# Optimization experiments

Measured on AMD Instinct MI355X. Metric: run time of the kernel, lower is better.

## Reference

```python
import jax, jax.numpy as jnp
import numpy as np

B, T_IN, T_OUT, F, H = 256, 336, 96, 32, 256


def _lstm_cell(x_t, h, c, Wih, Whh, b):
    # PyTorch gate order: input, forget, cell(g), output
    gates = x_t @ Wih.T + h @ Whh.T + b  # [B, 4H]
    i, f, g, o = jnp.split(gates, 4, axis=-1)
    c_new = jax.nn.sigmoid(f) * c + jax.nn.sigmoid(i) * jnp.tanh(g)
    h_new = jax.nn.sigmoid(o) * jnp.tanh(c_new)
    return h_new, c_new


def setup_inputs() -> dict:
    key = jax.random.key(0)
    ks = jax.random.split(key, 16)
    s = 0.05  # keep recurrence numerically tame
    g = lambda k, shape: (jax.random.normal(k, shape) * s).astype(jnp.float32)
    return {
        "x": jax.random.normal(ks[0], (B, T_IN, F), dtype=jnp.float32),
        "enc_Wih0": g(ks[1], (4 * H, F)),
        "enc_Whh0": g(ks[2], (4 * H, H)),
        "enc_b0": g(ks[3], (4 * H,)),
        "enc_Wih1": g(ks[4], (4 * H, H)),
        "enc_Whh1": g(ks[5], (4 * H, H)),
        "enc_b1": g(ks[6], (4 * H,)),
        "dec_Wih0": g(ks[7], (4 * H, F)),
        "dec_Whh0": g(ks[8], (4 * H, H)),
        "dec_b0": g(ks[9], (4 * H,)),
        "dec_Wih1": g(ks[10], (4 * H, H)),
        "dec_Whh1": g(ks[11], (4 * H, H)),
        "dec_b1": g(ks[12], (4 * H,)),
        "dec_Wout": g(ks[13], (F, H)),
        "dec_bout": g(ks[14], (F,)),
    }


def reference(x, enc_Wih0, enc_Whh0, enc_b0, enc_Wih1, enc_Whh1, enc_b1,
              dec_Wih0, dec_Whh0, dec_b0, dec_Wih1, dec_Whh1, dec_b1,
              dec_Wout, dec_bout):
    batch = x.shape[0]
    zeros = jnp.zeros((batch, H), dtype=x.dtype)

    # --- encoder: step-by-step 2-layer LSTM over input sequence ---
    def enc_step(carry, x_t):
        h0, c0, h1, c1 = carry
        h0, c0 = _lstm_cell(x_t, h0, c0, enc_Wih0, enc_Whh0, enc_b0)
        h1, c1 = _lstm_cell(h0, h1, c1, enc_Wih1, enc_Whh1, enc_b1)
        return (h0, c0, h1, c1), None

    xs = jnp.swapaxes(x, 0, 1)  # [T_IN, B, F]
    (h0, c0, h1, c1), _ = jax.lax.scan(enc_step, (zeros, zeros, zeros, zeros), xs)

    def dec_step(carry, _):
        h0, c0, h1, c1, y = carry
        h0, c0 = _lstm_cell(y, h0, c0, dec_Wih0, dec_Whh0, dec_b0)
        h1, c1 = _lstm_cell(h0, h1, c1, dec_Wih1, dec_Whh1, dec_b1)
        y = h1 @ dec_Wout.T + dec_bout  # project hidden -> feature dim
        return (h0, c0, h1, c1, y), y

    y0 = x[:, -1, :]  # [B, F]
    _, ys = jax.lax.scan(dec_step, (h0, c0, h1, c1, y0), None, length=T_OUT)
    return jnp.swapaxes(ys, 0, 1)  # [B, T_OUT, F]
```

## Files before the change

kernel.cpp:

```cpp
#include <hip/hip_runtime.h>
#include <hip/hip_bf16.h>

#define BB   256
#define TIN  336
#define TOUT 96
#define FF   32
#define HH   256

#define NGS 16
#define NBG 16
#define RPG 16
#define TPB 512

#define KB0 9
#define KB1 16
#define ASTRIDE 520
#define XSTRIDE 40

#define N_L0  (16*4*KB0*64*8)
#define N_L1  (16*4*KB1*64*8)
#define U_E0  0
#define U_E1  (U_E0 + N_L0)
#define U_D0  (U_E1 + N_L1)
#define U_D1  (U_D0 + N_L1)
#define U_END (U_D1 + N_L1)
#define HPAR  65536
#define U_H0  U_END
#define U_H1  (U_H0 + 2*HPAR)
#define U_HD  (U_H1 + 2*HPAR)
#define U_CTR (U_HD + 96*HPAR)
#define U_ZEND (U_CTR + 2048)

#define GATE(bias, g, r, cc) (bias[(g)*16 + (cc)] + pbuf[0][r][(g)*16 + (cc)] + pbuf[1][r][(g)*16 + (cc)])

typedef __bf16 bf16x8 __attribute__((ext_vector_type(8)));
typedef float  f32x4  __attribute__((ext_vector_type(4)));

__device__ __forceinline__ float sigf(float x) { return 1.f / (1.f + __expf(-x)); }
__device__ __forceinline__ float tanhfast(float x) { return 1.f - 2.f / (__expf(2.f * x) + 1.f); }
__device__ __forceinline__ unsigned short f2bf(float f) {
    union { float f; unsigned u; } v; v.f = f;
    unsigned r = v.u + 0x7FFF + ((v.u >> 16) & 1);
    return (unsigned short)(r >> 16);
}
__device__ __forceinline__ uint4 ldg_sc(const void* p) {
    uint4 v;
    asm volatile("global_load_dwordx4 %0, %1, off sc0 sc1\n\ts_waitcnt vmcnt(0)"
                 : "=v"(v) : "v"(p) : "memory");
    return v;
}
__device__ __forceinline__ void ldg_sc2(const void* p0, const void* p1, uint4& a, uint4& b) {
    asm volatile("global_load_dwordx4 %0, %2, off sc0 sc1\n\t"
                 "global_load_dwordx4 %1, %3, off sc0 sc1\n\t"
                 "s_waitcnt vmcnt(0)"
                 : "=v"(a), "=v"(b) : "v"(p0), "v"(p1) : "memory");
}

__global__ void prep_kernel(const float* __restrict__ eWih0, const float* __restrict__ eWhh0,
                            const float* __restrict__ eWih1, const float* __restrict__ eWhh1,
                            const float* __restrict__ dWih0, const float* __restrict__ dWhh0,
                            const float* __restrict__ dWih1, const float* __restrict__ dWhh1,
                            const float* __restrict__ Wout,  float* __restrict__ wsf)
{
    unsigned short* wsu = (unsigned short*)wsf;
    for (long u = (long)blockIdx.x * blockDim.x + threadIdx.x; u < (long)U_END;
         u += (long)gridDim.x * blockDim.x) {
        int region; long l;
        if (u < U_E1)      { region = 0; l = u - U_E0; }
        else if (u < U_D0) { region = 1; l = u - U_E1; }
        else if (u < U_D1) { region = 2; l = u - U_D0; }
        else               { region = 3; l = u - U_D1; }
        const int KB = (region == 0) ? KB0 : KB1;
        int j = (int)(l & 7), lane = (int)((l >> 3) & 63);
        long rem = l >> 9;
        int kb = (int)(rem % KB), q = (int)(rem / KB);
        int nt = q & 3, gi = q >> 2;
        int k  = kb * 32 + ((lane >> 4) << 3) + j;
        int gj = nt * 256 + gi * 16 + (lane & 15);
        float v;
        if (region == 0)      v = (k < 32)  ? eWih0[gj * 32 + k]  : eWhh0[gj * 256 + (k - 32)];
        else if (region == 1) v = (k < 256) ? eWih1[gj * 256 + k] : eWhh1[gj * 256 + (k - 256)];
        else if (region == 2) {
            if (k < 256) v = dWhh0[gj * 256 + k];
            else {
                float acc = 0.f; int kk = k - 256;
                #pragma unroll 8
                for (int f = 0; f < 32; ++f) acc += dWih0[gj * 32 + f] * Wout[f * 256 + kk];
                v = acc;
            }
        } else                v = (k < 256) ? dWih1[gj * 256 + k] : dWhh1[gj * 256 + (k - 256)];
        wsu[u] = f2bf(v);
    }
    for (long z = (long)blockIdx.x * blockDim.x + threadIdx.x; z < (long)(4 * HPAR);
         z += (long)gridDim.x * blockDim.x)
        wsu[U_H0 + z] = 0;
    for (long z = (long)blockIdx.x * blockDim.x + threadIdx.x; z < 2048;
         z += (long)gridDim.x * blockDim.x)
        wsu[U_CTR + z] = 0;
}

__global__ __launch_bounds__(TPB) void lstm_main(
    const float* __restrict__ x,
    const float* __restrict__ eb0, const float* __restrict__ eb1,
    const float* __restrict__ db0, const float* __restrict__ db1,
    const float* __restrict__ Wout, const float* __restrict__ bout,
    const float* __restrict__ dWih0,
    float* __restrict__ ws, float* __restrict__ out)
{
    const int gi = blockIdx.x >> 4;
    const int gb = blockIdx.x & 15;

    unsigned short* wsu = (unsigned short*)ws;
    const unsigned short* h0u = wsu + U_H0;
    const unsigned short* h1u = wsu + U_H1;
    const unsigned short* hdu = wsu + U_HD;
    unsigned* h0d = (unsigned*)(wsu + U_H0);
    unsigned* hdd = (unsigned*)(wsu + U_HD);
    unsigned* flg = (unsigned*)(wsu + U_CTR) + gb * 32;

    const int t  = threadIdx.x;
    const int wv = t >> 6;
    const int ln = t & 63;
    const int nt = wv & 3, w2 = wv >> 2;
    const int arow = ln & 15, ak = (ln >> 4) << 3;

    __shared__ __align__(16) unsigned short Atile[16 * ASTRIDE];
    __shared__ __align__(16) unsigned short Xtile[16 * XSTRIDE];
    __shared__ float pbuf[2][16][68];
    __shared__ float cst[2][16][16];
    __shared__ float sb[5][64];

    if (t < 64) {
        int gj = (t >> 4) * 256 + gi * 16 + (t & 15);
        sb[0][t] = eb0[gj]; sb[1][t] = eb1[gj]; sb[3][t] = db1[gj]; sb[4][t] = db0[gj];
        float be = db0[gj];
        #pragma unroll 8
        for (int f = 0; f < 32; ++f) be += dWih0[gj * 32 + f] * bout[f];
        sb[2][t] = be;
    }
    if (t < 256) { cst[0][t >> 4][t & 15] = 0.f; cst[1][t >> 4][t & 15] = 0.f; }

    bf16x8 B0[8], B1[8];
    const int kbs0 = w2 ? 4 : 0, kbn0 = w2 ? 5 : 4;
    const int kbs1 = w2 ? 8 : 0;
    auto loadB = [&](size_t ubase, int KB, int kbs, int kbn, bf16x8* Breg) {
        #pragma unroll
        for (int i = 0; i < 8; ++i)
            if (i < kbn)
                Breg[i] = *(const bf16x8*)(wsu + ubase +
                            ((size_t)(nt * KB + kbs + i) * 64 + ln) * 8);
    };

    int posts = 0;
    auto gsync = [&]() {
        ++posts;
        if (t == 0)
            __hip_atomic_store(flg + gi, (unsigned)posts, __ATOMIC_RELAXED,
                               __HIP_MEMORY_SCOPE_AGENT);
        if (wv == 0) {
            for (;;) {
                unsigned v = __hip_atomic_load(flg + (ln & 15), __ATOMIC_RELAXED,
                                               __HIP_MEMORY_SCOPE_AGENT);
                if (__all((int)(v >= (unsigned)posts))) break;
                __builtin_amdgcn_s_sleep(1);
            }
        }
        __syncthreads();
    };

    auto stageEnc = [&](const unsigned short* h0src, const unsigned short* h1src, int xs) {
        const int r = t >> 5, c8 = t & 31;
        uint4 a, b;
        ldg_sc2(h0src + (size_t)(gb * RPG + r) * 256 + c8 * 8,
                h1src + (size_t)(gb * RPG + r) * 256 + c8 * 8, a, b);
        float xv = 0.f;
        if (xs >= 0) xv = x[((size_t)(gb * RPG + r) * TIN + xs) * FF + c8];
        *(uint4*)(Atile + r * ASTRIDE + c8 * 8) = a;
        *(uint4*)(Atile + r * ASTRIDE + 256 + c8 * 8) = b;
        if (xs >= 0) Xtile[r * XSTRIDE + c8] = f2bf(xv);
    };
    auto stageOne = [&](const unsigned short* src, int colbase) {
        const int r = t >> 5, c8 = t & 31;
        uint4 a = ldg_sc(src + (size_t)(gb * RPG + r) * 256 + c8 * 8);
        *(uint4*)(Atile + r * ASTRIDE + colbase + c8 * 8) = a;
    };
    auto stageTwo = [&](const unsigned short* s0, int cb0, const unsigned short* s1, int cb1) {
        const int r = t >> 5, c8 = t & 31;
        uint4 a, b;
        ldg_sc2(s0 + (size_t)(gb * RPG + r) * 256 + c8 * 8,
                s1 + (size_t)(gb * RPG + r) * 256 + c8 * 8, a, b);
        *(uint4*)(Atile + r * ASTRIDE + cb0 + c8 * 8) = a;
        *(uint4*)(Atile + r * ASTRIDE + cb1 + c8 * 8) = b;
    };
    auto stageZero = [&](int colbase) {
        const int r = t >> 5, c8 = t & 31;
        uint4 z = {0u, 0u, 0u, 0u};
        *(uint4*)(Atile + r * ASTRIDE + colbase + c8 * 8) = z;
    };

    auto phase = [&](const bf16x8* Breg, int kbs, int kbn, bool withX, const float* bias,
                     int layer, unsigned* hdstDw, bool addY0) {
        f32x4 acc = {0.f, 0.f, 0.f, 0.f};
        #pragma unroll
        for (int i = 0; i < 8; ++i) {
            if (i < kbn) {
                const int kb = kbs + i;
                bf16x8 a;
                if (withX && kb == 0) a = *(const bf16x8*)(Xtile + arow * XSTRIDE + ak);
                else {
                    const int koff = (withX ? (kb - 1) : kb) * 32;
                    a = *(const bf16x8*)(Atile + arow * ASTRIDE + koff + ak);
                }
                acc = __builtin_amdgcn_mfma_f32_16x16x32_bf16(a, Breg[i], acc, 0, 0, 0);
            }
        }
        #pragma unroll
        for (int rg = 0; rg < 4; ++rg)
            pbuf[w2][(ln >> 4) * 4 + rg][nt * 16 + arow] = acc[rg];
        __syncthreads();
        if (t < 128) {
            const int r = t >> 3, c2 = t & 7;
            const int c0 = c2 * 2, c1 = c0 + 1;
            float xi0 = GATE(bias, 0, r, c0), xf0 = GATE(bias, 1, r, c0);
            float xg0 = GATE(bias, 2, r, c0), xo0 = GATE(bias, 3, r, c0);
            float xi1 = GATE(bias, 0, r, c1), xf1 = GATE(bias, 1, r, c1);
            float xg1 = GATE(bias, 2, r, c1), xo1 = GATE(bias, 3, r, c1);
            if (addY0) {
                const float* xp = x + ((size_t)(gb * RPG + r) * TIN + (TIN - 1)) * FF;
                float xr[32];
                #pragma unroll
                for (int f = 0; f < 32; ++f) xr[f] = xp[f];
                #pragma unroll
                for (int g = 0; g < 4; ++g) {
                    const float* w0 = dWih0 + (size_t)(g * 256 + gi * 16 + c0) * 32;
                    const float* w1 = dWih0 + (size_t)(g * 256 + gi * 16 + c1) * 32;
                    float a0 = 0.f, a1 = 0.f;
                    #pragma unroll
                    for (int f = 0; f < 32; ++f) {
                        a0 = fmaf(w0[f], xr[f], a0);
                        a1 = fmaf(w1[f], xr[f], a1);
                    }
                    if (g == 0) { xi0 += a0; xi1 += a1; }
                    else if (g == 1) { xf0 += a0; xf1 += a1; }
                    else if (g == 2) { xg0 += a0; xg1 += a1; }
                    else { xo0 += a0; xo1 += a1; }
                }
            }
            float ca = cst[layer][r][c0], cb = cst[layer][r][c1];
            float cn0 = sigf(xf0) * ca + sigf(xi0) * tanhfast(xg0);
            float cn1 = sigf(xf1) * cb + sigf(xi1) * tanhfast(xg1);
            cst[layer][r][c0] = cn0; cst[layer][r][c1] = cn1;
            float h0v = sigf(xo0) * tanhfast(cn0);
            float h1v = sigf(xo1) * tanhfast(cn1);
            unsigned pv = (unsigned)f2bf(h0v) | ((unsigned)f2bf(h1v) << 16);
            __hip_atomic_store(hdstDw + (size_t)(gb * RPG + r) * 128 + gi * 8 + c2, pv,
                               __ATOMIC_RELAXED, __HIP_MEMORY_SCOPE_AGENT);
        }
        __syncthreads();
    };

    loadB(U_E0 + (size_t)gi * 18432, KB0, kbs0, kbn0, B0);
    loadB(U_E1 + (size_t)gi * 32768, KB1, kbs1, 8,    B1);
    { const int r = t >> 5, c8 = t & 31;
      uint4 z = {0u, 0u, 0u, 0u};
      *(uint4*)(Atile + r * ASTRIDE + c8 * 8) = z;
      Xtile[r * XSTRIDE + c8] = f2bf(x[((size_t)(gb * RPG + r) * TIN) * FF + c8]); }
    __syncthreads();

    for (int s = 0; s < TIN; ++s) {
        const int rp = s & 1, wp = rp ^ 1;
        phase(B0, kbs0, kbn0, true, sb[0], 0, h0d + (size_t)wp * (HPAR / 2), false);
        gsync();
        stageEnc(h0u + (size_t)wp * HPAR, h1u + (size_t)rp * HPAR,
                 (s + 1 < TIN) ? s + 1 : -1);
        __syncthreads();
        phase(B1, kbs1, 8, false, sb[1], 1,
              (unsigned*)(wsu + U_H1) + (size_t)wp * (HPAR / 2), false);
    }

    loadB(U_D0 + (size_t)gi * 32768, KB1, kbs1, 8, B0);
    loadB(U_D1 + (size_t)gi * 32768, KB1, kbs1, 8, B1);

    for (int s = TIN; s < TIN + TOUT; ++s) {
        const int wp = (s & 1) ^ 1, td = s - TIN;
        gsync();
        if (td == 0) stageZero(256);
        else stageOne(hdu + (size_t)(td - 1) * HPAR, 256);
        __syncthreads();
        phase(B0, kbs1, 8, false, (td == 0) ? sb[4] : sb[2], 0,
              h0d + (size_t)wp * (HPAR / 2), td == 0);
        gsync();
        if (td == 0) stageTwo(h0u + (size_t)wp * HPAR, 0, h1u + 0 * HPAR, 256);
        else stageOne(h0u + (size_t)wp * HPAR, 0);
        __syncthreads();
        phase(B1, kbs1, 8, false, sb[3], 1, hdd + (size_t)td * (HPAR / 2), false);
    }

    gsync();

    {
        const int r = t >> 5, fq = (t >> 4) & 1, kc = t & 15;
        const int f = gi * 2 + fq;
        const float* wf = Wout + (size_t)f * 256 + kc * 16;
        float wreg[16];
        #pragma unroll
        for (int i = 0; i < 16; ++i) wreg[i] = wf[i];
        const float bo = bout[f];
        for (int td = 0; td < TOUT; ++td) {
            const unsigned short* hp = hdu + (size_t)td * HPAR +
                                       (size_t)(gb * RPG + r) * 256 + kc * 16;
            uint4 ua = *(const uint4*)hp;
            uint4 ub = *(const uint4*)(hp + 8);
            unsigned w[8] = {ua.x, ua.y, ua.z, ua.w, ub.x, ub.y, ub.z, ub.w};
            float a = 0.f;
            #pragma unroll
            for (int j = 0; j < 8; ++j) {
                a = fmaf(__uint_as_float(w[j] << 16),        wreg[2 * j],     a);
                a = fmaf(__uint_as_float(w[j] & 0xffff0000u), wreg[2 * j + 1], a);
            }
            #pragma unroll
            for (int off = 1; off < 16; off <<= 1) a += __shfl_xor(a, off, 64);
            if (kc == 0)
                out[((size_t)(gb * RPG + r) * TOUT + td) * FF + f] = a + bo;
        }
    }
}

extern "C" void kernel_launch(void* const* d_in, const int* in_sizes, int n_in,
                              void* d_out, int out_size, void* d_ws, size_t ws_size,
                              hipStream_t stream) {
    const float* x     = (const float*)d_in[0];
    const float* eWih0 = (const float*)d_in[1];
    const float* eWhh0 = (const float*)d_in[2];
    const float* eb0   = (const float*)d_in[3];
    const float* eWih1 = (const float*)d_in[4];
    const float* eWhh1 = (const float*)d_in[5];
    const float* eb1   = (const float*)d_in[6];
    const float* dWih0 = (const float*)d_in[7];
    const float* dWhh0 = (const float*)d_in[8];
    const float* db0   = (const float*)d_in[9];
    const float* dWih1 = (const float*)d_in[10];
    const float* dWhh1 = (const float*)d_in[11];
    const float* db1   = (const float*)d_in[12];
    const float* dWout = (const float*)d_in[13];
    const float* dbout = (const float*)d_in[14];
    float* ws = (float*)d_ws;
    float* out = (float*)d_out;

    prep_kernel<<<1024, 256, 0, stream>>>(eWih0, eWhh0, eWih1, eWhh1,
                                          dWih0, dWhh0, dWih1, dWhh1, dWout, ws);
    lstm_main<<<NGS * NBG, TPB, 0, stream>>>(x, eb0, eb1, db0, db1,
                                             dWout, dbout, dWih0, ws, out);
}
```

Before: 1.497 ms.

## Replace flag barriers with step-tagged hidden-state words polled directly by consumers

New measurement: 1.930 ms. +28.9%, slower.

```diff
diff --git a/kernel.cpp b/kernel.cpp
--- a/kernel.cpp
+++ b/kernel.cpp
@@ -24,17 +24,21 @@
 #define U_D0  (U_E1 + N_L1)
 #define U_D1  (U_D0 + N_L1)
 #define U_END (U_D1 + N_L1)
-#define HPAR  65536
+
+#define HPAR2 131072
+#define HU    32768
 #define U_H0  U_END
-#define U_H1  (U_H0 + 2*HPAR)
-#define U_HD  (U_H1 + 2*HPAR)
-#define U_CTR (U_HD + 96*HPAR)
-#define U_ZEND (U_CTR + 2048)
+#define U_H1  (U_H0 + 2*HPAR2)
+#define U_HD  (U_H1 + 2*HPAR2)
+#define U_ZEND (U_HD + 2*HPAR2)
+
+#define POLL_CAP (1 << 22)
 
 #define GATE(bias, g, r, cc) (bias[(g)*16 + (cc)] + pbuf[0][r][(g)*16 + (cc)] + pbuf[1][r][(g)*16 + (cc)])
 
 typedef __bf16 bf16x8 __attribute__((ext_vector_type(8)));
 typedef float  f32x4  __attribute__((ext_vector_type(4)));
+typedef unsigned long long u64;
 
 __device__ __forceinline__ float sigf(float x) { return 1.f / (1.f + __expf(-x)); }
 __device__ __forceinline__ float tanhfast(float x) { return 1.f - 2.f / (__expf(2.f * x) + 1.f); }
@@ -42,18 +46,6 @@
     union { float f; unsigned u; } v; v.f = f;
     unsigned r = v.u + 0x7FFF + ((v.u >> 16) & 1);
     return (unsigned short)(r >> 16);
-}
-__device__ __forceinline__ uint4 ldg_sc(const void* p) {
-    uint4 v;
-    asm volatile("global_load_dwordx4 %0, %1, off sc0 sc1\n\ts_waitcnt vmcnt(0)"
-                 : "=v"(v) : "v"(p) : "memory");
-    return v;
-}
-__device__ __forceinline__ void ldg_sc2(const void* p0, const void* p1, uint4& a, uint4& b) {
-    asm volatile("global_load_dwordx4 %0, %2, off sc0 sc1\n\t"
-                 "global_load_dwordx4 %1, %3, off sc0 sc1\n\t"
-                 "s_waitcnt vmcnt(0)"
-                 : "=v"(a), "=v"(b) : "v"(p0), "v"(p1) : "memory");
 }
 
 __global__ void prep_kernel(const float* __restrict__ eWih0, const float* __restrict__ eWhh0,
@@ -91,12 +83,9 @@
         } else                v = (k < 256) ? dWih1[gj * 256 + k] : dWhh1[gj * 256 + (k - 256)];
         wsu[u] = f2bf(v);
     }
-    for (long z = (long)blockIdx.x * blockDim.x + threadIdx.x; z < (long)(4 * HPAR);
+    for (long z = (long)blockIdx.x * blockDim.x + threadIdx.x; z < (long)(6 * HPAR2);
          z += (long)gridDim.x * blockDim.x)
         wsu[U_H0 + z] = 0;
-    for (long z = (long)blockIdx.x * blockDim.x + threadIdx.x; z < 2048;
-         z += (long)gridDim.x * blockDim.x)
-        wsu[U_CTR + z] = 0;
 }
 
 __global__ __launch_bounds__(TPB) void lstm_main(
@@ -111,12 +100,9 @@
     const int gb = blockIdx.x & 15;
 
     unsigned short* wsu = (unsigned short*)ws;
-    const unsigned short* h0u = wsu + U_H0;
-    const unsigned short* h1u = wsu + U_H1;
-    const unsigned short* hdu = wsu + U_HD;
-    unsigned* h0d = (unsigned*)(wsu + U_H0);
-    unsigned* hdd = (unsigned*)(wsu + U_HD);
-    unsigned* flg = (unsigned*)(wsu + U_CTR) + gb * 32;
+    u64* h0q = (u64*)(wsu + U_H0);
+    u64* h1q = (u64*)(wsu + U_H1);
+    u64* hdq = (u64*)(wsu + U_HD);
 
     const int t  = threadIdx.x;
     const int wv = t >> 6;
@@ -151,44 +137,51 @@
                             ((size_t)(nt * KB + kbs + i) * 64 + ln) * 8);
     };
 
-    int posts = 0;
-    auto gsync = [&]() {
-        ++posts;
-        if (t == 0)
-            __hip_atomic_store(flg + gi, (unsigned)posts, __ATOMIC_RELAXED,
-                               __HIP_MEMORY_SCOPE_AGENT);
-        if (wv == 0) {
-            for (;;) {
-                unsigned v = __hip_atomic_load(flg + (ln & 15), __ATOMIC_RELAXED,
-                                               __HIP_MEMORY_SCOPE_AGENT);
-                if (__all((int)(v >= (unsigned)posts))) break;
-                __builtin_amdgcn_s_sleep(1);
+    auto stageT = [&](const u64* src, int colbase, unsigned exp) {
+        const int r = t >> 5, c8 = t & 31;
+        const u64* p = src + (size_t)(gb * RPG + r) * 128 + c8 * 4;
+        u64 u0, u1, u2, u3;
+        int guard = 0;
+        for (;;) {
+            u0 = __hip_atomic_load(p + 0, __ATOMIC_RELAXED, __HIP_MEMORY_SCOPE_AGENT);
+            u1 = __hip_atomic_load(p + 1, __ATOMIC_RELAXED, __HIP_MEMORY_SCOPE_AGENT);
+            u2 = __hip_atomic_load(p + 2, __ATOMIC_RELAXED, __HIP_MEMORY_SCOPE_AGENT);
+            u3 = __hip_atomic_load(p + 3, __ATOMIC_RELAXED, __HIP_MEMORY_SCOPE_AGENT);
+            bool f = ((unsigned)(u0 >> 32) == exp) && ((unsigned)(u1 >> 32) == exp) &&
+                     ((unsigned)(u2 >> 32) == exp) && ((unsigned)(u3 >> 32) == exp);
+            if (__all((int)f)) break;
+            if (++guard > POLL_CAP) break;
+            __builtin_amdgcn_s_sleep(1);
+        }
+        uint4 a = {(unsigned)u0, (unsigned)u1, (unsigned)u2, (unsigned)u3};
+        *(uint4*)(Atile + r * ASTRIDE + colbase + c8 * 8) = a;
+    };
+    auto stageT2 = [&](const u64* s0, unsigned e0, int cb0,
+                       const u64* s1, unsigned e1, int cb1) {
+        const int r = t >> 5, c8 = t & 31;
+        const u64* p0 = s0 + (size_t)(gb * RPG + r) * 128 + c8 * 4;
+        const u64* p1 = s1 + (size_t)(gb * RPG + r) * 128 + c8 * 4;
+        u64 u[8];
+        int guard = 0;
+        for (;;) {
+            #pragma unroll
+            for (int k = 0; k < 4; ++k)
+                u[k]     = __hip_atomic_load(p0 + k, __ATOMIC_RELAXED, __HIP_MEMORY_SCOPE_AGENT);
+            #pragma unroll
+            for (int k = 0; k < 4; ++k)
+                u[4 + k] = __hip_atomic_load(p1 + k, __ATOMIC_RELAXED, __HIP_MEMORY_SCOPE_AGENT);
+            bool f = true;
+            #pragma unroll
+            for (int k = 0; k < 4; ++k) {
+                f = f && ((unsigned)(u[k] >> 32) == e0);
+                f = f && ((unsigned)(u[4 + k] >> 32) == e1);
             }
-        }
-        __syncthreads();
-    };
-
-    auto stageEnc = [&](const unsigned short* h0src, const unsigned short* h1src, int xs) {
-        const int r = t >> 5, c8 = t & 31;
-        uint4 a, b;
-        ldg_sc2(h0src + (size_t)(gb * RPG + r) * 256 + c8 * 8,
-                h1src + (size_t)(gb * RPG + r) * 256 + c8 * 8, a, b);
-        float xv = 0.f;
-        if (xs >= 0) xv = x[((size_t)(gb * RPG + r) * TIN + xs) * FF + c8];
-        *(uint4*)(Atile + r * ASTRIDE + c8 * 8) = a;
-        *(uint4*)(Atile + r * ASTRIDE + 256 + c8 * 8) = b;
-        if (xs >= 0) Xtile[r * XSTRIDE + c8] = f2bf(xv);
-    };
-    auto stageOne = [&](const unsigned short* src, int colbase) {
-        const int r = t >> 5, c8 = t & 31;
-        uint4 a = ldg_sc(src + (size_t)(gb * RPG + r) * 256 + c8 * 8);
-        *(uint4*)(Atile + r * ASTRIDE + colbase + c8 * 8) = a;
-    };
-    auto stageTwo = [&](const unsigned short* s0, int cb0, const unsigned short* s1, int cb1) {
-        const int r = t >> 5, c8 = t & 31;
-        uint4 a, b;
-        ldg_sc2(s0 + (size_t)(gb * RPG + r) * 256 + c8 * 8,
-                s1 + (size_t)(gb * RPG + r) * 256 + c8 * 8, a, b);
+            if (__all((int)f)) break;
+            if (++guard > POLL_CAP) break;
+            __builtin_amdgcn_s_sleep(1);
+        }
+        uint4 a = {(unsigned)u[0], (unsigned)u[1], (unsigned)u[2], (unsigned)u[3]};
+        uint4 b = {(unsigned)u[4], (unsigned)u[5], (unsigned)u[6], (unsigned)u[7]};
         *(uint4*)(Atile + r * ASTRIDE + cb0 + c8 * 8) = a;
         *(uint4*)(Atile + r * ASTRIDE + cb1 + c8 * 8) = b;
     };
@@ -197,9 +190,17 @@
         uint4 z = {0u, 0u, 0u, 0u};
         *(uint4*)(Atile + r * ASTRIDE + colbase + c8 * 8) = z;
     };
+    auto stageEnc = [&](const u64* h0src, unsigned e0, const u64* h1src, unsigned e1, int xs) {
+        stageT2(h0src, e0, 0, h1src, e1, 256);
+        if (xs >= 0) {
+            const int r = t >> 5, c8 = t & 31;
+            Xtile[r * XSTRIDE + c8] =
+                f2bf(x[((size_t)(gb * RPG + r) * TIN + xs) * FF + c8]);
+        }
+    };
 
     auto phase = [&](const bf16x8* Breg, int kbs, int kbn, bool withX, const float* bias,
-                     int layer, unsigned* hdstDw, bool addY0) {
+                     int layer, u64* hq, unsigned tag, bool addY0) {
         f32x4 acc = {0.f, 0.f, 0.f, 0.f};
         #pragma unroll
         for (int i = 0; i < 8; ++i) {
@@ -253,7 +254,8 @@
             float h0v = sigf(xo0) * tanhfast(cn0);
             float h1v = sigf(xo1) * tanhfast(cn1);
             unsigned pv = (unsigned)f2bf(h0v) | ((unsigned)f2bf(h1v) << 16);
-            __hip_atomic_store(hdstDw + (size_t)(gb * RPG + r) * 128 + gi * 8 + c2, pv,
+            u64 uv = ((u64)tag << 32) | (u64)pv;
+            __hip_atomic_store(hq + (size_t)(gb * RPG + r) * 128 + gi * 8 + c2, uv,
                                __ATOMIC_RELAXED, __HIP_MEMORY_SCOPE_AGENT);
         }
         __syncthreads();
@@ -269,61 +271,57 @@
 
     for (int s = 0; s < TIN; ++s) {
         const int rp = s & 1, wp = rp ^ 1;
-        phase(B0, kbs0, kbn0, true, sb[0], 0, h0d + (size_t)wp * (HPAR / 2), false);
-        gsync();
-        stageEnc(h0u + (size_t)wp * HPAR, h1u + (size_t)rp * HPAR,
+        phase(B0, kbs0, kbn0, true, sb[0], 0, h0q + (size_t)wp * HU, (unsigned)(s + 1), false);
+        stageEnc(h0q + (size_t)wp * HU, (unsigned)(s + 1),
+                 h1q + (size_t)rp * HU, (unsigned)s,
                  (s + 1 < TIN) ? s + 1 : -1);
         __syncthreads();
-        phase(B1, kbs1, 8, false, sb[1], 1,
-              (unsigned*)(wsu + U_H1) + (size_t)wp * (HPAR / 2), false);
+        phase(B1, kbs1, 8, false, sb[1], 1, h1q + (size_t)wp * HU, (unsigned)(s + 1), false);
     }
 
     loadB(U_D0 + (size_t)gi * 32768, KB1, kbs1, 8, B0);
     loadB(U_D1 + (size_t)gi * 32768, KB1, kbs1, 8, B1);
-
-    for (int s = TIN; s < TIN + TOUT; ++s) {
-        const int wp = (s & 1) ^ 1, td = s - TIN;
-        gsync();
+    const int yr = t >> 5, yfq = (t >> 4) & 1, ykc = t & 15;
+    const int yf = gi * 2 + yfq;
+    float wreg[16];
+    #pragma unroll
+    for (int i = 0; i < 16; ++i) wreg[i] = Wout[(size_t)yf * 256 + ykc * 16 + i];
+    const float ybo = bout[yf];
+    auto ycompute = [&](int td) {
+        const unsigned* ap = (const unsigned*)(Atile + yr * ASTRIDE + 256 + ykc * 16);
+        float a = 0.f;
+        #pragma unroll
+        for (int j = 0; j < 8; ++j) {
+            unsigned w = ap[j];
+            a = fmaf(__uint_as_float(w << 16),         wreg[2 * j],     a);
+            a = fmaf(__uint_as_float(w & 0xffff0000u), wreg[2 * j + 1], a);
+        }
+        #pragma unroll
+        for (int off = 1; off < 16; off <<= 1) a += __shfl_xor(a, off, 64);
+        if (ykc == 0)
+            out[((size_t)(gb * RPG + yr) * TOUT + td) * FF + yf] = a + ybo;
+    };
+
+    for (int td = 0; td < TOUT; ++td) {
+        const int s = TIN + td;
+        const int wp = (s & 1) ^ 1;
         if (td == 0) stageZero(256);
-        else stageOne(hdu + (size_t)(td - 1) * HPAR, 256);
-        __syncthreads();
+        else stageT(hdq + (size_t)((td - 1) & 1) * HU, 256, (unsigned)s);
+        __syncthreads();
+        if (td > 0) ycompute(td - 1);
         phase(B0, kbs1, 8, false, (td == 0) ? sb[4] : sb[2], 0,
-              h0d + (size_t)wp * (HPAR / 2), td == 0);
-        gsync();
-        if (td == 0) stageTwo(h0u + (size_t)wp * HPAR, 0, h1u + 0 * HPAR, 256);
-        else stageOne(h0u + (size_t)wp * HPAR, 0);
-        __syncthreads();
-        phase(B1, kbs1, 8, false, sb[3], 1, hdd + (size_t)td * (HPAR / 2), false);
+              h0q + (size_t)wp * HU, (unsigned)(s + 1), td == 0);
+        if (td == 0) stageT2(h0q + (size_t)wp * HU, (unsigned)(s + 1), 0,
+                             h1q , (unsigned)TIN, 256);
+        else stageT(h0q + (size_t)wp * HU, 0, (unsigned)(s + 1));
+        __syncthreads();
+        phase(B1, kbs1, 8, false, sb[3], 1,
+              hdq + (size_t)(td & 1) * HU, (unsigned)(s + 1), false);
     }
 
-    gsync();
-
-    {
-        const int r = t >> 5, fq = (t >> 4) & 1, kc = t & 15;
-        const int f = gi * 2 + fq;
-        const float* wf = Wout + (size_t)f * 256 + kc * 16;
-        float wreg[16];
-        #pragma unroll
-        for (int i = 0; i < 16; ++i) wreg[i] = wf[i];
-        const float bo = bout[f];
-        for (int td = 0; td < TOUT; ++td) {
-            const unsigned short* hp = hdu + (size_t)td * HPAR +
-                                       (size_t)(gb * RPG + r) * 256 + kc * 16;
-            uint4 ua = *(const uint4*)hp;
-            uint4 ub = *(const uint4*)(hp + 8);
-            unsigned w[8] = {ua.x, ua.y, ua.z, ua.w, ub.x, ub.y, ub.z, ub.w};
-            float a = 0.f;
-            #pragma unroll
-            for (int j = 0; j < 8; ++j) {
-                a = fmaf(__uint_as_float(w[j] << 16),        wreg[2 * j],     a);
-                a = fmaf(__uint_as_float(w[j] & 0xffff0000u), wreg[2 * j + 1], a);
-            }
-            #pragma unroll
-            for (int off = 1; off < 16; off <<= 1) a += __shfl_xor(a, off, 64);
-            if (kc == 0)
-                out[((size_t)(gb * RPG + r) * TOUT + td) * FF + f] = a + bo;
-        }
-    }
+    stageT(hdq + (size_t)((TOUT - 1) & 1) * HU, 256, (unsigned)(TIN + TOUT));
+    __syncthreads();
+    ycompute(TOUT - 1);
 }
 
 extern "C" void kernel_launch(void* const* d_in, const int* in_sizes, int n_in,
```

## Poll grid barrier in every wave and fuse decoder output projection into loop

Applied to the files above, without the earlier changes.

New measurement: 2.110 ms. 1.41x slower.

```diff
diff --git a/kernel.cpp b/kernel.cpp
--- a/kernel.cpp
+++ b/kernel.cpp
@@ -28,7 +28,7 @@
 #define U_H0  U_END
 #define U_H1  (U_H0 + 2*HPAR)
 #define U_HD  (U_H1 + 2*HPAR)
-#define U_CTR (U_HD + 96*HPAR)
+#define U_CTR (U_HD + 2*HPAR)
 #define U_ZEND (U_CTR + 2048)
 
 #define GATE(bias, g, r, cc) (bias[(g)*16 + (cc)] + pbuf[0][r][(g)*16 + (cc)] + pbuf[1][r][(g)*16 + (cc)])
@@ -115,6 +115,7 @@
     const unsigned short* h1u = wsu + U_H1;
     const unsigned short* hdu = wsu + U_HD;
     unsigned* h0d = (unsigned*)(wsu + U_H0);
+    unsigned* h1d = (unsigned*)(wsu + U_H1);
     unsigned* hdd = (unsigned*)(wsu + U_HD);
     unsigned* flg = (unsigned*)(wsu + U_CTR) + gb * 32;
 
@@ -152,54 +153,21 @@
     };
 
     int posts = 0;
-    auto gsync = [&]() {
+    auto gpoll = [&]() {
         ++posts;
         if (t == 0)
             __hip_atomic_store(flg + gi, (unsigned)posts, __ATOMIC_RELAXED,
                                __HIP_MEMORY_SCOPE_AGENT);
-        if (wv == 0) {
-            for (;;) {
-                unsigned v = __hip_atomic_load(flg + (ln & 15), __ATOMIC_RELAXED,
-                                               __HIP_MEMORY_SCOPE_AGENT);
-                if (__all((int)(v >= (unsigned)posts))) break;
-                __builtin_amdgcn_s_sleep(1);
-            }
-        }
-        __syncthreads();
+        for (;;) {
+            unsigned v = __hip_atomic_load(flg + (ln & 15), __ATOMIC_RELAXED,
+                                           __HIP_MEMORY_SCOPE_AGENT);
+            if (__all((int)(v >= (unsigned)posts))) break;
+            __builtin_amdgcn_s_sleep(1);
+        }
     };
 
-    auto stageEnc = [&](const unsigned short* h0src, const unsigned short* h1src, int xs) {
-        const int r = t >> 5, c8 = t & 31;
-        uint4 a, b;
-        ldg_sc2(h0src + (size_t)(gb * RPG + r) * 256 + c8 * 8,
-                h1src + (size_t)(gb * RPG + r) * 256 + c8 * 8, a, b);
-        float xv = 0.f;
-        if (xs >= 0) xv = x[((size_t)(gb * RPG + r) * TIN + xs) * FF + c8];
-        *(uint4*)(Atile + r * ASTRIDE + c8 * 8) = a;
-        *(uint4*)(Atile + r * ASTRIDE + 256 + c8 * 8) = b;
-        if (xs >= 0) Xtile[r * XSTRIDE + c8] = f2bf(xv);
-    };
-    auto stageOne = [&](const unsigned short* src, int colbase) {
-        const int r = t >> 5, c8 = t & 31;
-        uint4 a = ldg_sc(src + (size_t)(gb * RPG + r) * 256 + c8 * 8);
-        *(uint4*)(Atile + r * ASTRIDE + colbase + c8 * 8) = a;
-    };
-    auto stageTwo = [&](const unsigned short* s0, int cb0, const unsigned short* s1, int cb1) {
-        const int r = t >> 5, c8 = t & 31;
-        uint4 a, b;
-        ldg_sc2(s0 + (size_t)(gb * RPG + r) * 256 + c8 * 8,
-                s1 + (size_t)(gb * RPG + r) * 256 + c8 * 8, a, b);
-        *(uint4*)(Atile + r * ASTRIDE + cb0 + c8 * 8) = a;
-        *(uint4*)(Atile + r * ASTRIDE + cb1 + c8 * 8) = b;
-    };
-    auto stageZero = [&](int colbase) {
-        const int r = t >> 5, c8 = t & 31;
-        uint4 z = {0u, 0u, 0u, 0u};
-        *(uint4*)(Atile + r * ASTRIDE + colbase + c8 * 8) = z;
-    };
-
     auto phase = [&](const bf16x8* Breg, int kbs, int kbn, bool withX, const float* bias,
-                     int layer, unsigned* hdstDw, bool addY0) {
+                     int layer, unsigned* hdstDw, bool addY0, bool drain) {
         f32x4 acc = {0.f, 0.f, 0.f, 0.f};
         #pragma unroll
         for (int i = 0; i < 8; ++i) {
@@ -256,6 +224,7 @@
             __hip_atomic_store(hdstDw + (size_t)(gb * RPG + r) * 128 + gi * 8 + c2, pv,
                                __ATOMIC_RELAXED, __HIP_MEMORY_SCOPE_AGENT);
         }
+        if (drain) asm volatile("s_waitcnt vmcnt(0)" : : : "memory");
         __syncthreads();
     };
 
@@ -269,61 +238,97 @@
 
     for (int s = 0; s < TIN; ++s) {
         const int rp = s & 1, wp = rp ^ 1;
-        phase(B0, kbs0, kbn0, true, sb[0], 0, h0d + (size_t)wp * (HPAR / 2), false);
-        gsync();
-        stageEnc(h0u + (size_t)wp * HPAR, h1u + (size_t)rp * HPAR,
-                 (s + 1 < TIN) ? s + 1 : -1);
-        __syncthreads();
-        phase(B1, kbs1, 8, false, sb[1], 1,
-              (unsigned*)(wsu + U_H1) + (size_t)wp * (HPAR / 2), false);
+        phase(B0, kbs0, kbn0, true, sb[0], 0, h0d + (size_t)wp * (HPAR / 2), false, true);
+        {
+            const int r = t >> 5, c8 = t & 31;
+            const int xs = (s + 1 < TIN) ? s + 1 : -1;
+            float xv = 0.f;
+            if (xs >= 0) xv = x[((size_t)(gb * RPG + r) * TIN + xs) * FF + c8];
+            gpoll();
+            uint4 a, b;
+            ldg_sc2(h0u + (size_t)wp * HPAR + (size_t)(gb * RPG + r) * 256 + c8 * 8,
+                    h1u + (size_t)rp * HPAR + (size_t)(gb * RPG + r) * 256 + c8 * 8, a, b);
+            *(uint4*)(Atile + r * ASTRIDE + c8 * 8) = a;
+            *(uint4*)(Atile + r * ASTRIDE + 256 + c8 * 8) = b;
+            if (xs >= 0) Xtile[r * XSTRIDE + c8] = f2bf(xv);
+            __syncthreads();
+        }
+        phase(B1, kbs1, 8, false, sb[1], 1, h1d + (size_t)wp * (HPAR / 2),
+              false, s == TIN - 1);
     }
 
     loadB(U_D0 + (size_t)gi * 32768, KB1, kbs1, 8, B0);
     loadB(U_D1 + (size_t)gi * 32768, KB1, kbs1, 8, B1);
-
-    for (int s = TIN; s < TIN + TOUT; ++s) {
-        const int wp = (s & 1) ^ 1, td = s - TIN;
-        gsync();
-        if (td == 0) stageZero(256);
-        else stageOne(hdu + (size_t)(td - 1) * HPAR, 256);
+    const int yr = t >> 5, yfq = (t >> 4) & 1, ykc = t & 15;
+    const int yf = gi * 2 + yfq;
+    float wreg[16];
+    #pragma unroll
+    for (int i = 0; i < 16; ++i) wreg[i] = Wout[(size_t)yf * 256 + ykc * 16 + i];
+    const float ybo = bout[yf];
+    auto ycompute = [&](int td) {
+        const unsigned* ap = (const unsigned*)(Atile + yr * ASTRIDE + 256 + ykc * 16);
+        float a = 0.f;
+        #pragma unroll
+        for (int j = 0; j < 8; ++j) {
+            unsigned w = ap[j];
+            a = fmaf(__uint_as_float(w << 16),         wreg[2 * j],     a);
+            a = fmaf(__uint_as_float(w & 0xffff0000u), wreg[2 * j + 1], a);
+        }
+        #pragma unroll
+        for (int off = 1; off < 16; off <<= 1) a += __shfl_xor(a, off, 64);
+        if (ykc == 0)
+            out[((size_t)(gb * RPG + yr) * TOUT + td) * FF + yf] = a + ybo;
+    };
+
+    for (int td = 0; td < TOUT; ++td) {
+        const int s = TIN + td;
+        const int wp = (s & 1) ^ 1;
+        {
+            const int r = t >> 5, c8 = t & 31;
+            gpoll();
+            if (td == 0) {
+                uint4 z = {0u, 0u, 0u, 0u};
+                *(uint4*)(Atile + r * ASTRIDE + 256 + c8 * 8) = z;
+            } else {
+                uint4 a = ldg_sc(hdu + (size_t)((td - 1) & 1) * HPAR +
+                                 (size_t)(gb * RPG + r) * 256 + c8 * 8);
+                *(uint4*)(Atile + r * ASTRIDE + 256 + c8 * 8) = a;
+            }
+            __syncthreads();
+        }
+        if (td > 0) ycompute(td - 1);
+        phase(B0, kbs1, 8, false, (td == 0) ? sb[4] : sb[2], 0,
+              h0d + (size_t)wp * (HPAR / 2), td == 0, true);
+        {
+            const int r = t >> 5, c8 = t & 31;
+            gpoll();
+            if (td == 0) {
+                uint4 a, b;
+                ldg_sc2(h0u + (size_t)wp * HPAR + (size_t)(gb * RPG + r) * 256 + c8 * 8,
+                        h1u + 0 * HPAR  + (size_t)(gb * RPG + r) * 256 + c8 * 8,
+                        a, b);
+                *(uint4*)(Atile + r * ASTRIDE + c8 * 8) = a;
+                *(uint4*)(Atile + r * ASTRIDE + 256 + c8 * 8) = b;
+            } else {
+                uint4 a = ldg_sc(h0u + (size_t)wp * HPAR +
+                                 (size_t)(gb * RPG + r) * 256 + c8 * 8);
+                *(uint4*)(Atile + r * ASTRIDE + c8 * 8) = a;
+            }
+            __syncthreads();
+        }
+        phase(B1, kbs1, 8, false, sb[3], 1, hdd + (size_t)(td & 1) * (HPAR / 2),
+              false, true);
+    }
+
+    {
+        const int r = t >> 5, c8 = t & 31;
+        gpoll();
+        uint4 a = ldg_sc(hdu + (size_t)((TOUT - 1) & 1) * HPAR +
+                         (size_t)(gb * RPG + r) * 256 + c8 * 8);
+        *(uint4*)(Atile + r * ASTRIDE + 256 + c8 * 8) = a;
         __syncthreads();
-        phase(B0, kbs1, 8, false, (td == 0) ? sb[4] : sb[2], 0,
-              h0d + (size_t)wp * (HPAR / 2), td == 0);
-        gsync();
-        if (td == 0) stageTwo(h0u + (size_t)wp * HPAR, 0, h1u + 0 * HPAR, 256);
-        else stageOne(h0u + (size_t)wp * HPAR, 0);
-        __syncthreads();
-        phase(B1, kbs1, 8, false, sb[3], 1, hdd + (size_t)td * (HPAR / 2), false);
-    }
-
-    gsync();
-
-    {
-        const int r = t >> 5, fq = (t >> 4) & 1, kc = t & 15;
-        const int f = gi * 2 + fq;
-        const float* wf = Wout + (size_t)f * 256 + kc * 16;
-        float wreg[16];
-        #pragma unroll
-        for (int i = 0; i < 16; ++i) wreg[i] = wf[i];
-        const float bo = bout[f];
-        for (int td = 0; td < TOUT; ++td) {
-            const unsigned short* hp = hdu + (size_t)td * HPAR +
-                                       (size_t)(gb * RPG + r) * 256 + kc * 16;
-            uint4 ua = *(const uint4*)hp;
-            uint4 ub = *(const uint4*)(hp + 8);
-            unsigned w[8] = {ua.x, ua.y, ua.z, ua.w, ub.x, ub.y, ub.z, ub.w};
-            float a = 0.f;
-            #pragma unroll
-            for (int j = 0; j < 8; ++j) {
-                a = fmaf(__uint_as_float(w[j] << 16),        wreg[2 * j],     a);
-                a = fmaf(__uint_as_float(w[j] & 0xffff0000u), wreg[2 * j + 1], a);
-            }
-            #pragma unroll
-            for (int off = 1; off < 16; off <<= 1) a += __shfl_xor(a, off, 64);
-            if (kc == 0)
-                out[((size_t)(gb * RPG + r) * TOUT + td) * FF + f] = a + bo;
-        }
-    }
+    }
+    ycompute(TOUT - 1);
 }
 
 extern "C" void kernel_launch(void* const* d_in, const int* in_sizes, int n_in,
```
